# Kernel tuning notes

Hardware: AMD Instinct MI355X
Metric: run time of the kernel (lower is better)

Reference implementation:

```python
import jax, jax.numpy as jnp
import numpy as np

B, C, T = 524288, 10, 25

def setup_inputs() -> dict:
    key = jax.random.key(0)
    k1, k2, k3, k4 = jax.random.split(key, 4)
    mu = jax.random.normal(k1, (B, C), dtype=jnp.float32)
    log_sigma2 = jax.random.normal(k2, (B, C), dtype=jnp.float32)
    y = jax.random.randint(k3, (B,), 0, C, dtype=jnp.int64)
    # MVN(0, I) sample == iid standard normal noise, shape [T, B, C]
    eps = jax.random.normal(k4, (T, B, C), dtype=jnp.float32)
    return {"mu": mu, "log_sigma2": log_sigma2, "y": y, "eps": eps}

def reference(mu, log_sigma2, y, eps):
    T_ = eps.shape[0]
    # reparameterized logits: [T, B, C]
    logits = mu[None, :, :] + jnp.exp(0.5 * log_sigma2)[None, :, :] * eps
    # log_softmax over classes, minus log(T)
    logp = jax.nn.log_softmax(logits, axis=-1) - jnp.log(jnp.float32(T_))
    # logsumexp over the T MC samples -> [B, C]
    lse = jax.scipy.special.logsumexp(logp, axis=0)
    # nll_loss: mean of -log p(y)
    picked = jnp.take_along_axis(lse, y[:, None].astype(jnp.int32), axis=1)[:, 0]
    return -jnp.mean(picked)
```

## Files before the change

### kernel.cpp

```cpp
#include <hip/hip_runtime.h>
#include <math.h>

#define BB 524288
#define CC 10
#define TT 25

__global__ void init_out_kernel(float* out) {
    *out = logf((float)TT);
}

__global__ __launch_bounds__(256) void mc_nll_kernel(
    const float* __restrict__ mu,
    const float* __restrict__ ls2,
    const int*   __restrict__ y,
    const float* __restrict__ eps,
    float* __restrict__ out)
{
    const int b = blockIdx.x * blockDim.x + threadIdx.x;

    float muv[CC], sig[CC];
    const float2* mu2 = reinterpret_cast<const float2*>(mu  + (size_t)b * CC);
    const float2* ls22 = reinterpret_cast<const float2*>(ls2 + (size_t)b * CC);
#pragma unroll
    for (int i = 0; i < CC / 2; ++i) {
        float2 m2 = mu2[i];
        float2 s2 = ls22[i];
        muv[2 * i]     = m2.x;
        muv[2 * i + 1] = m2.y;
        sig[2 * i]     = __expf(0.5f * s2.x);
        sig[2 * i + 1] = __expf(0.5f * s2.y);
    }
    const int yi = y[b];

    float M = -INFINITY, S = 0.0f;
    for (int t = 0; t < TT; ++t) {
        const float2* e2 = reinterpret_cast<const float2*>(
            eps + ((size_t)t * BB + (size_t)b) * CC);
        float l[CC];
#pragma unroll
        for (int i = 0; i < CC / 2; ++i) {
            float2 e = e2[i];
            l[2 * i]     = fmaf(sig[2 * i],     e.x, muv[2 * i]);
            l[2 * i + 1] = fmaf(sig[2 * i + 1], e.y, muv[2 * i + 1]);
        }
        float m = -INFINITY;
        float ly = 0.0f;
#pragma unroll
        for (int c = 0; c < CC; ++c) {
            m = fmaxf(m, l[c]);
            ly = (c == yi) ? l[c] : ly;
        }
        float s = 0.0f;
#pragma unroll
        for (int c = 0; c < CC; ++c) s += __expf(l[c] - m);
        const float v = ly - (m + __logf(s));

        const float nm = fmaxf(M, v);
        S = S * __expf(M - nm) + __expf(v - nm);
        M = nm;
    }
    const float picked_no_logT = M + __logf(S);

    float x = picked_no_logT;
#pragma unroll
    for (int off = 32; off > 0; off >>= 1)
        x += __shfl_down(x, off, 64);

    __shared__ float wsum[4];
    const int lane = threadIdx.x & 63;
    const int wid  = threadIdx.x >> 6;
    if (lane == 0) wsum[wid] = x;
    __syncthreads();
    if (threadIdx.x == 0) {
        float bs = wsum[0] + wsum[1] + wsum[2] + wsum[3];
        atomicAdd(out, -bs * (1.0f / (float)BB));
    }
}

extern "C" void kernel_launch(void* const* d_in, const int* in_sizes, int n_in,
                              void* d_out, int out_size, void* d_ws, size_t ws_size,
                              hipStream_t stream) {
    const float* mu  = (const float*)d_in[0];
    const float* ls2 = (const float*)d_in[1];
    const int*   y   = (const int*)d_in[2];
    const float* eps = (const float*)d_in[3];
    float* out = (float*)d_out;

    hipLaunchKernelGGL(init_out_kernel, dim3(1), dim3(1), 0, stream, out);
    hipLaunchKernelGGL(mc_nll_kernel, dim3(BB / 256), dim3(256), 0, stream,
                       mu, ls2, y, eps, out);
}
```

Baseline: 104.3 us.

## Stage eps and mu/logsigma tiles into LDS via async global_load_lds double buffering

Replaces per-thread strided float2 global loads of eps, mu and log_sigma2 with coalesced 16-byte global_load_lds copies into shared memory. The eps slabs for two time steps are double-buffered so the next pair loads while the current pair is computed. The last time step still reads directly from global memory. This targets the poorly coalesced 40-byte-stride accesses and exposed load latency, at the cost of 40KB LDS per block (lower occupancy), extra barriers and hand-written waitcnt synchronisation.

```diff
diff --git a/kernel.cpp b/kernel.cpp
--- a/kernel.cpp
+++ b/kernel.cpp
@@ -4,6 +4,14 @@
 #define BB 524288
 #define CC 10
 #define TT 25
+#define BLK 256
+#define SLAB (BLK * CC)
+#define HALF (SLAB / 2)
+
+#define GLL16(src, dst)                                                     \
+    __builtin_amdgcn_global_load_lds(                                       \
+        (const __attribute__((address_space(1))) void*)(src),               \
+        (__attribute__((address_space(3))) void*)(dst), 16, 0, 0)
 
 __global__ void init_out_kernel(float* out) {
     *out = logf((float)TT);
@@ -16,26 +24,105 @@
     const float* __restrict__ eps,
     float* __restrict__ out)
 {
-    const int b = blockIdx.x * blockDim.x + threadIdx.x;
+    __shared__ float lds[2][2 * SLAB];
+    __shared__ float wsum[4];
+
+    const int tid  = threadIdx.x;
+    const int wid  = tid >> 6;
+    const int lane = tid & 63;
+    const int G    = blockIdx.x * BLK;
+    const int b    = G + tid;
+
+    const int yi = y[b];
+
+    {
+        const float* base = (wid >> 1) ? ls2 : mu;
+        const float* src  = base + (size_t)G * CC + (wid & 1) * HALF + lane * 4;
+        float*       dst  = &lds[1][(wid >> 1) * SLAB + (wid & 1) * HALF];
+#pragma unroll
+        for (int j = 0; j < 5; ++j)
+            GLL16(src + j * 256, dst + j * 256);
+    }
+
+    {
+        const int t = (wid >> 1);
+        const float* src = eps + ((size_t)t * BB + G) * CC + (wid & 1) * HALF + lane * 4;
+        float*       dst = &lds[0][(wid >> 1) * SLAB + (wid & 1) * HALF];
+#pragma unroll
+        for (int j = 0; j < 5; ++j)
+            GLL16(src + j * 256, dst + j * 256);
+    }
+
+    asm volatile("s_waitcnt vmcnt(5)" ::: "memory");
+    __builtin_amdgcn_s_barrier();
 
     float muv[CC], sig[CC];
-    const float2* mu2 = reinterpret_cast<const float2*>(mu  + (size_t)b * CC);
-    const float2* ls22 = reinterpret_cast<const float2*>(ls2 + (size_t)b * CC);
+    {
+        const float* mrow = &lds[1][tid * CC];
+        const float* srow = &lds[1][SLAB + tid * CC];
 #pragma unroll
-    for (int i = 0; i < CC / 2; ++i) {
-        float2 m2 = mu2[i];
-        float2 s2 = ls22[i];
-        muv[2 * i]     = m2.x;
-        muv[2 * i + 1] = m2.y;
-        sig[2 * i]     = __expf(0.5f * s2.x);
-        sig[2 * i + 1] = __expf(0.5f * s2.y);
+        for (int i = 0; i < CC / 2; ++i) {
+            float2 m2 = *reinterpret_cast<const float2*>(mrow + 2 * i);
+            float2 s2 = *reinterpret_cast<const float2*>(srow + 2 * i);
+            muv[2 * i]     = m2.x;
+            muv[2 * i + 1] = m2.y;
+            sig[2 * i]     = __expf(0.5f * s2.x);
+            sig[2 * i + 1] = __expf(0.5f * s2.y);
+        }
     }
-    const int yi = y[b];
+    asm volatile("s_waitcnt lgkmcnt(0)" ::: "memory");
+    __builtin_amdgcn_s_barrier();
 
     float M = -INFINITY, S = 0.0f;
-    for (int t = 0; t < TT; ++t) {
+    int buf = 0;
+    for (int p = 0; p < 12; ++p) {
+        if (p < 11) {
+            const int t = 2 * (p + 1) + (wid >> 1);
+            const float* src = eps + ((size_t)t * BB + G) * CC + (wid & 1) * HALF + lane * 4;
+            float*       dst = &lds[buf ^ 1][(wid >> 1) * SLAB + (wid & 1) * HALF];
+#pragma unroll
+            for (int j = 0; j < 5; ++j)
+                GLL16(src + j * 256, dst + j * 256);
+            asm volatile("s_waitcnt vmcnt(5)" ::: "memory");
+        } else {
+            asm volatile("s_waitcnt vmcnt(0)" ::: "memory");
+        }
+        __builtin_amdgcn_s_barrier();
+
+#pragma unroll
+        for (int ti = 0; ti < 2; ++ti) {
+            const float* row = &lds[buf][ti * SLAB + tid * CC];
+            float l[CC];
+#pragma unroll
+            for (int i = 0; i < CC / 2; ++i) {
+                float2 e = *reinterpret_cast<const float2*>(row + 2 * i);
+                l[2 * i]     = fmaf(sig[2 * i],     e.x, muv[2 * i]);
+                l[2 * i + 1] = fmaf(sig[2 * i + 1], e.y, muv[2 * i + 1]);
+            }
+            float m = -INFINITY, ly = 0.0f;
+#pragma unroll
+            for (int c = 0; c < CC; ++c) {
+                m = fmaxf(m, l[c]);
+                ly = (c == yi) ? l[c] : ly;
+            }
+            float s = 0.0f;
+#pragma unroll
+            for (int c = 0; c < CC; ++c) s += __expf(l[c] - m);
+            const float v = ly - (m + __logf(s));
+
+            const float nm = fmaxf(M, v);
+            S = S * __expf(M - nm) + __expf(v - nm);
+            M = nm;
+        }
+
+        asm volatile("s_waitcnt lgkmcnt(0)" ::: "memory");
+        __builtin_amdgcn_s_barrier();
+        buf ^= 1;
+    }
+
+    {
         const float2* e2 = reinterpret_cast<const float2*>(
-            eps + ((size_t)t * BB + (size_t)b) * CC);
+            eps + ((size_t)24 * BB + (size_t)b) * CC);
         float l[CC];
 #pragma unroll
         for (int i = 0; i < CC / 2; ++i) {
@@ -43,8 +130,7 @@
             l[2 * i]     = fmaf(sig[2 * i],     e.x, muv[2 * i]);
             l[2 * i + 1] = fmaf(sig[2 * i + 1], e.y, muv[2 * i + 1]);
         }
-        float m = -INFINITY;
-        float ly = 0.0f;
+        float m = -INFINITY, ly = 0.0f;
 #pragma unroll
         for (int c = 0; c < CC; ++c) {
             m = fmaxf(m, l[c]);
@@ -54,7 +140,6 @@
 #pragma unroll
         for (int c = 0; c < CC; ++c) s += __expf(l[c] - m);
         const float v = ly - (m + __logf(s));
-
         const float nm = fmaxf(M, v);
         S = S * __expf(M - nm) + __expf(v - nm);
         M = nm;
@@ -66,12 +151,9 @@
     for (int off = 32; off > 0; off >>= 1)
         x += __shfl_down(x, off, 64);
 
-    __shared__ float wsum[4];
-    const int lane = threadIdx.x & 63;
-    const int wid  = threadIdx.x >> 6;
     if (lane == 0) wsum[wid] = x;
     __syncthreads();
-    if (threadIdx.x == 0) {
+    if (tid == 0) {
         float bs = wsum[0] + wsum[1] + wsum[2] + wsum[3];
         atomicAdd(out, -bs * (1.0f / (float)BB));
     }
@@ -87,6 +169,6 @@
     float* out = (float*)d_out;
 
     hipLaunchKernelGGL(init_out_kernel, dim3(1), dim3(1), 0, stream, out);
-    hipLaunchKernelGGL(mc_nll_kernel, dim3(BB / 256), dim3(256), 0, stream,
+    hipLaunchKernelGGL(mc_nll_kernel, dim3(BB / BLK), dim3(BLK), 0, stream,
                        mu, ls2, y, eps, out);
 }
```

After: 113.3 us. +8.6%, slower.

## Process two rows per thread with float4 loads, double-buffered eps, direct prob sum

Applied to the files above, without the earlier changes.

Each thread now handles two batch rows, so all loads become 16-byte float4 vectors, and eps slabs are double-buffered across MC samples to overlap loads with math. The online logsumexp over T is replaced by directly summing softmax probabilities (exp(l_y-m)/sum) and taking one log at the end. This removes per-sample log/exp rescaling. The trade-off is more register pressure and slightly different numerics, since probabilities are summed without a max shift.

```diff
diff --git a/kernel.cpp b/kernel.cpp
--- a/kernel.cpp
+++ b/kernel.cpp
@@ -4,6 +4,10 @@
 #define BB 524288
 #define CC 10
 #define TT 25
+#define BLK 256
+#define NPAIR (BB / 2)
+#define NBLK (NPAIR / BLK)
+#define SLABF (BB * CC)
 
 __global__ void init_out_kernel(float* out) {
     *out = logf((float)TT);
@@ -16,52 +20,81 @@
     const float* __restrict__ eps,
     float* __restrict__ out)
 {
-    const int b = blockIdx.x * blockDim.x + threadIdx.x;
+    const int i = blockIdx.x * BLK + threadIdx.x;
+    const size_t base = (size_t)i * (2 * CC);
 
-    float muv[CC], sig[CC];
-    const float2* mu2 = reinterpret_cast<const float2*>(mu  + (size_t)b * CC);
-    const float2* ls22 = reinterpret_cast<const float2*>(ls2 + (size_t)b * CC);
+    const int2 yy  = *reinterpret_cast<const int2*>(y + 2 * i);
+    const int  yi0 = yy.x, yi1 = yy.y;
+
+    float muv[2 * CC], sig[2 * CC];
+    {
+        const float4* m4 = reinterpret_cast<const float4*>(mu + base);
+        const float4* s4 = reinterpret_cast<const float4*>(ls2 + base);
 #pragma unroll
-    for (int i = 0; i < CC / 2; ++i) {
-        float2 m2 = mu2[i];
-        float2 s2 = ls22[i];
-        muv[2 * i]     = m2.x;
-        muv[2 * i + 1] = m2.y;
-        sig[2 * i]     = __expf(0.5f * s2.x);
-        sig[2 * i + 1] = __expf(0.5f * s2.y);
+        for (int j = 0; j < 5; ++j) {
+            float4 m = m4[j];
+            float4 s = s4[j];
+            muv[4 * j + 0] = m.x; muv[4 * j + 1] = m.y;
+            muv[4 * j + 2] = m.z; muv[4 * j + 3] = m.w;
+            sig[4 * j + 0] = __expf(0.5f * s.x);
+            sig[4 * j + 1] = __expf(0.5f * s.y);
+            sig[4 * j + 2] = __expf(0.5f * s.z);
+            sig[4 * j + 3] = __expf(0.5f * s.w);
+        }
     }
-    const int yi = y[b];
 
-    float M = -INFINITY, S = 0.0f;
-    for (int t = 0; t < TT; ++t) {
-        const float2* e2 = reinterpret_cast<const float2*>(
-            eps + ((size_t)t * BB + (size_t)b) * CC);
-        float l[CC];
+    float S0 = 0.0f, S1 = 0.0f;
+    const float* ebase = eps + base;
+
+    auto compute = [&](const float4 (&e)[5]) {
+        float l[2 * CC];
 #pragma unroll
-        for (int i = 0; i < CC / 2; ++i) {
-            float2 e = e2[i];
-            l[2 * i]     = fmaf(sig[2 * i],     e.x, muv[2 * i]);
-            l[2 * i + 1] = fmaf(sig[2 * i + 1], e.y, muv[2 * i + 1]);
+        for (int j = 0; j < 5; ++j) {
+            l[4 * j + 0] = fmaf(sig[4 * j + 0], e[j].x, muv[4 * j + 0]);
+            l[4 * j + 1] = fmaf(sig[4 * j + 1], e[j].y, muv[4 * j + 1]);
+            l[4 * j + 2] = fmaf(sig[4 * j + 2], e[j].z, muv[4 * j + 2]);
+            l[4 * j + 3] = fmaf(sig[4 * j + 3], e[j].w, muv[4 * j + 3]);
         }
-        float m = -INFINITY;
-        float ly = 0.0f;
+        float m0 = l[0], m1 = l[CC];
+#pragma unroll
+        for (int c = 1; c < CC; ++c) {
+            m0 = fmaxf(m0, l[c]);
+            m1 = fmaxf(m1, l[CC + c]);
+        }
+        float s0 = 0.0f, s1 = 0.0f, e0 = 0.0f, e1 = 0.0f;
 #pragma unroll
         for (int c = 0; c < CC; ++c) {
-            m = fmaxf(m, l[c]);
-            ly = (c == yi) ? l[c] : ly;
+            float x0 = __expf(l[c] - m0);
+            float x1 = __expf(l[CC + c] - m1);
+            s0 += x0; s1 += x1;
+            e0 = (c == yi0) ? x0 : e0;
+            e1 = (c == yi1) ? x1 : e1;
         }
-        float s = 0.0f;
-#pragma unroll
-        for (int c = 0; c < CC; ++c) s += __expf(l[c] - m);
-        const float v = ly - (m + __logf(s));
+        S0 = fmaf(e0, __builtin_amdgcn_rcpf(s0), S0);
+        S1 = fmaf(e1, __builtin_amdgcn_rcpf(s1), S1);
+    };
 
-        const float nm = fmaxf(M, v);
-        S = S * __expf(M - nm) + __expf(v - nm);
-        M = nm;
+#define LOADE(buf, t)                                                          \
+    {                                                                          \
+        const float4* p =                                                      \
+            reinterpret_cast<const float4*>(ebase + (size_t)(t) * SLABF);      \
+        _Pragma("unroll") for (int j = 0; j < 5; ++j) (buf)[j] = p[j];         \
     }
-    const float picked_no_logT = M + __logf(S);
 
-    float x = picked_no_logT;
+    float4 eA[5], eB[5];
+    LOADE(eA, 0);
+    for (int p = 0; p < 12; ++p) {
+        const int t = 2 * p;
+        LOADE(eB, t + 1);
+        compute(eA);
+        LOADE(eA, t + 2);
+        compute(eB);
+    }
+    compute(eA);
+
+    const float picked2 = __logf(S0) + __logf(S1);
+
+    float x = picked2;
 #pragma unroll
     for (int off = 32; off > 0; off >>= 1)
         x += __shfl_down(x, off, 64);
@@ -87,6 +120,6 @@
     float* out = (float*)d_out;
 
     hipLaunchKernelGGL(init_out_kernel, dim3(1), dim3(1), 0, stream, out);
-    hipLaunchKernelGGL(mc_nll_kernel, dim3(BB / 256), dim3(256), 0, stream,
+    hipLaunchKernelGGL(mc_nll_kernel, dim3(NBLK), dim3(BLK), 0, stream,
                        mu, ls2, y, eps, out);
 }
```

Measured after the change: 117.5 us. 1.13x slower.

## Stage eps through LDS with async global_load_lds and simplify softmax accumulation

Applied to the files above, without the earlier changes.

Each wave now copies its contiguous eps slab for the next sample into double-buffered LDS with global_load_lds, which gives coalesced 16-byte loads instead of strided per-thread float2 loads. Samples are read back from LDS while the next slab is in flight. The per-sample log-softmax and online logsumexp are replaced by a direct sum of softmax probabilities (exp_y/sum) with a single log at the end, cutting the exp and log count. The risks are the hand-written waitcnt synchronisation and some precision loss, since the probabilities are summed without max-rescaling across samples.

```diff
diff --git a/kernel.cpp b/kernel.cpp
--- a/kernel.cpp
+++ b/kernel.cpp
@@ -4,6 +4,15 @@
 #define BB 524288
 #define CC 10
 #define TT 25
+#define BLK 256
+#define NBLK (BB / BLK)
+#define WSLAB (64 * CC)
+#define SLABF ((size_t)BB * CC)
+
+#define GLL(src, dst, n)                                                    \
+    __builtin_amdgcn_global_load_lds(                                       \
+        (const __attribute__((address_space(1))) void*)(src),               \
+        (__attribute__((address_space(3))) void*)(dst), n, 0, 0)
 
 __global__ void init_out_kernel(float* out) {
     *out = logf((float)TT);
@@ -16,62 +25,85 @@
     const float* __restrict__ eps,
     float* __restrict__ out)
 {
-    const int b = blockIdx.x * blockDim.x + threadIdx.x;
+    __shared__ float slab[2][4][WSLAB];
+    __shared__ float wsum[4];
+
+    const int tid  = threadIdx.x;
+    const int wid  = tid >> 6;
+    const int lane = tid & 63;
+    const int b    = blockIdx.x * BLK + tid;
+
+    const int yi = y[b];
 
     float muv[CC], sig[CC];
-    const float2* mu2 = reinterpret_cast<const float2*>(mu  + (size_t)b * CC);
-    const float2* ls22 = reinterpret_cast<const float2*>(ls2 + (size_t)b * CC);
+    {
+        const float2* m2 = reinterpret_cast<const float2*>(mu  + (size_t)b * CC);
+        const float2* s2 = reinterpret_cast<const float2*>(ls2 + (size_t)b * CC);
 #pragma unroll
-    for (int i = 0; i < CC / 2; ++i) {
-        float2 m2 = mu2[i];
-        float2 s2 = ls22[i];
-        muv[2 * i]     = m2.x;
-        muv[2 * i + 1] = m2.y;
-        sig[2 * i]     = __expf(0.5f * s2.x);
-        sig[2 * i + 1] = __expf(0.5f * s2.y);
+        for (int i = 0; i < CC / 2; ++i) {
+            float2 m = m2[i];
+            float2 s = s2[i];
+            muv[2 * i]     = m.x;
+            muv[2 * i + 1] = m.y;
+            sig[2 * i]     = __expf(0.5f * s.x);
+            sig[2 * i + 1] = __expf(0.5f * s.y);
+        }
     }
-    const int yi = y[b];
 
-    float M = -INFINITY, S = 0.0f;
+    const float* wbase = eps + (size_t)blockIdx.x * BLK * CC + wid * WSLAB;
+
+    auto stage = [&](int t, int bf) {
+        const float* s = wbase + (size_t)t * SLABF;
+        float*       d = &slab[bf][wid][0];
+        GLL(s + 4 * lane,        d,        16);
+        GLL(s + 256 + 4 * lane,  d + 256,  16);
+        GLL(s + 512 + lane,      d + 512,  4);
+        GLL(s + 576 + lane,      d + 576,  4);
+    };
+
+    stage(0, 0);
+
+    float S  = 0.0f;
+    int   bf = 0;
     for (int t = 0; t < TT; ++t) {
-        const float2* e2 = reinterpret_cast<const float2*>(
-            eps + ((size_t)t * BB + (size_t)b) * CC);
+        asm volatile("s_waitcnt lgkmcnt(0)" ::: "memory");
+        if (t < TT - 1) {
+            stage(t + 1, bf ^ 1);
+            asm volatile("s_waitcnt vmcnt(4)" ::: "memory");
+        } else {
+            asm volatile("s_waitcnt vmcnt(0)" ::: "memory");
+        }
+
+        const float* row = &slab[bf][wid][lane * CC];
         float l[CC];
 #pragma unroll
         for (int i = 0; i < CC / 2; ++i) {
-            float2 e = e2[i];
+            float2 e = *reinterpret_cast<const float2*>(row + 2 * i);
             l[2 * i]     = fmaf(sig[2 * i],     e.x, muv[2 * i]);
             l[2 * i + 1] = fmaf(sig[2 * i + 1], e.y, muv[2 * i + 1]);
         }
-        float m = -INFINITY;
-        float ly = 0.0f;
+        float m = l[0];
+#pragma unroll
+        for (int c = 1; c < CC; ++c) m = fmaxf(m, l[c]);
+        float s = 0.0f, ey = 0.0f;
 #pragma unroll
         for (int c = 0; c < CC; ++c) {
-            m = fmaxf(m, l[c]);
-            ly = (c == yi) ? l[c] : ly;
+            float x = __expf(l[c] - m);
+            s += x;
+            ey = (c == yi) ? x : ey;
         }
-        float s = 0.0f;
-#pragma unroll
-        for (int c = 0; c < CC; ++c) s += __expf(l[c] - m);
-        const float v = ly - (m + __logf(s));
+        S = fmaf(ey, __builtin_amdgcn_rcpf(s), S);
+        bf ^= 1;
+    }
 
-        const float nm = fmaxf(M, v);
-        S = S * __expf(M - nm) + __expf(v - nm);
-        M = nm;
-    }
-    const float picked_no_logT = M + __logf(S);
-
-    float x = picked_no_logT;
+    float x = __logf(S);
 #pragma unroll
     for (int off = 32; off > 0; off >>= 1)
         x += __shfl_down(x, off, 64);
 
-    __shared__ float wsum[4];
-    const int lane = threadIdx.x & 63;
-    const int wid  = threadIdx.x >> 6;
     if (lane == 0) wsum[wid] = x;
     __syncthreads();
-    if (threadIdx.x == 0) {
+    if (tid == 0) {
         float bs = wsum[0] + wsum[1] + wsum[2] + wsum[3];
         atomicAdd(out, -bs * (1.0f / (float)BB));
     }
@@ -87,6 +119,6 @@
     float* out = (float*)d_out;
 
     hipLaunchKernelGGL(init_out_kernel, dim3(1), dim3(1), 0, stream, out);
-    hipLaunchKernelGGL(mc_nll_kernel, dim3(BB / 256), dim3(256), 0, stream,
+    hipLaunchKernelGGL(mc_nll_kernel, dim3(NBLK), dim3(BLK), 0, stream,
                        mu, ls2, y, eps, out);
 }
```

After: 109.9 us. 1.05x slower.
